# Kernel tuning notes

Measured on AMD Instinct MI355X. Metric: run time of the kernel, lower is better.

## Reference

```python
import jax, jax.numpy as jnp
import numpy as np
import math

T, B, E, H = 1024, 4, 512, 8
HD = E // H

def setup_inputs() -> dict:
    key = jax.random.key(0)
    ks = jax.random.split(key, 6)
    return {
        "query": jax.random.normal(ks[0], (T, B, E), dtype=jnp.float32),
        "dist": jax.random.normal(ks[1], (B, T, T, H), dtype=jnp.float32) * 0.1,
        "in_proj_weight": jax.random.normal(ks[2], (3 * E, E), dtype=jnp.float32) * 0.02,
        "in_proj_bias": jax.random.normal(ks[3], (3 * E,), dtype=jnp.float32) * 0.02,
        "out_proj_weight": jax.random.normal(ks[4], (E, E), dtype=jnp.float32) * 0.02,
        "out_proj_bias": jax.random.normal(ks[5], (E,), dtype=jnp.float32) * 0.02,
    }

def reference(query, dist, in_proj_weight, in_proj_bias, out_proj_weight, out_proj_bias):
    t, b, e = query.shape
    # packed in-projection (self-attention: q=k=v=query)
    qkv = query @ in_proj_weight.T + in_proj_bias          # [T,B,3E]
    q, k, v = jnp.split(qkv, 3, axis=-1)                   # each [T,B,E]
    def heads(x):
        return x.reshape(t, b * H, HD).transpose(1, 0, 2)  # [B*H,T,HD]
    q, k, v = heads(q), heads(k), heads(v)
    q = q / math.sqrt(HD)
    attn = jnp.einsum('bte,bse->bts', q, k)                # [B*H,T,T]
    # distance/structure bias: [B,T,T,H] -> [B,H,T,T] -> [B*H,T,T]
    bias = jnp.transpose(dist, (0, 3, 1, 2)).reshape(b * H, t, t)
    attn = jax.nn.softmax(attn + bias, axis=-1)
    out = jnp.einsum('bts,bse->bte', attn, v)              # [B*H,T,HD]
    out = out.transpose(1, 0, 2).reshape(t, b, e)          # [T,B,E]
    out = out @ out_proj_weight.T + out_proj_bias
    return out
```

## Files before the change

kernel.cpp:

```cpp
#include <hip/hip_runtime.h>
#include <math.h>

typedef __bf16 bf16;
typedef bf16 bf16x8 __attribute__((ext_vector_type(8)));
typedef bf16 bf16x4 __attribute__((ext_vector_type(4)));
typedef float f32x4 __attribute__((ext_vector_type(4)));

#define T_DIM 1024
#define B_DIM 4
#define E_DIM 512
#define H_DIM 8
#define HD_DIM 64
#define BH_DIM 32

__device__ __forceinline__ f32x4 mfma16(bf16x8 a, bf16x8 b, f32x4 c) {
    return __builtin_amdgcn_mfma_f32_16x16x32_bf16(a, b, c, 0, 0, 0);
}

__device__ __forceinline__ bf16x4 cvt4(f32x4 v) {
    bf16x4 o;
    o[0] = (bf16)v[0]; o[1] = (bf16)v[1]; o[2] = (bf16)v[2]; o[3] = (bf16)v[3];
    return o;
}

__global__ __launch_bounds__(256)
void bias_transpose(const float* __restrict__ dist, bf16* __restrict__ bias_t) {
    const int bt = blockIdx.x;
    const int b = bt >> 10, t = bt & 1023;
    const float* src = dist + ((long)bt << 13);
    const int tid = threadIdx.x;
#pragma unroll
    for (int rep = 0; rep < 4; rep++) {
        int slot = rep * 256 + tid;
        int h = slot >> 7;
        int sc = (slot & 127) * 8;
        bf16x8 o;
#pragma unroll
        for (int i = 0; i < 8; i++)
            o[i] = (bf16)src[(sc + i) * 8 + h];
        *(bf16x8*)&bias_t[((long)(b * 8 + h) * T_DIM + t) * T_DIM + sc] = o;
    }
}

template<int TM, int TN, int MODE>
__global__ __launch_bounds__(256)
void gemm_t(const float* __restrict__ A, const float* __restrict__ Bt,
            const float* __restrict__ bias, int K, int N,
            float* __restrict__ out, bf16* __restrict__ qb,
            bf16* __restrict__ kb, bf16* __restrict__ vb) {
    constexpr int FM = TM / 32, FN = TN / 32;
    __shared__ __align__(16) bf16 As[TM * 72];
    __shared__ __align__(16) bf16 Bs[TN * 72];
    const int tid  = threadIdx.x;
    const int lane = tid & 63;
    const int wave = tid >> 6;
    const int quad = lane >> 4;
    const int l15  = lane & 15;
    const int wm = wave & 1, wn = wave >> 1;
    const int m0 = blockIdx.x * TM, n0 = blockIdx.y * TN;

    f32x4 acc[FM][FN] = {};

    const int sr = tid >> 2;
    const int sc = (tid & 3) * 16;

    for (int k0 = 0; k0 < K; k0 += 64) {
#pragma unroll
        for (int p = 0; p < TM / 64; p++) {
            const float* src = &A[(long)(m0 + p * 64 + sr) * K + k0 + sc];
#pragma unroll
            for (int j = 0; j < 4; j++)
                *(bf16x4*)&As[(p * 64 + sr) * 72 + sc + j * 4] =
                    cvt4(*(const f32x4*)(src + j * 4));
        }
#pragma unroll
        for (int p = 0; p < TN / 64; p++) {
            const float* src = &Bt[(long)(n0 + p * 64 + sr) * K + k0 + sc];
#pragma unroll
            for (int j = 0; j < 4; j++)
                *(bf16x4*)&Bs[(p * 64 + sr) * 72 + sc + j * 4] =
                    cvt4(*(const f32x4*)(src + j * 4));
        }
        __syncthreads();
#pragma unroll
        for (int kk = 0; kk < 64; kk += 32) {
            bf16x8 af[FM], bf[FN];
#pragma unroll
            for (int mb = 0; mb < FM; mb++)
                af[mb] = *(const bf16x8*)&As[(wm * (TM / 2) + mb * 16 + l15) * 72 + kk + quad * 8];
#pragma unroll
            for (int nb = 0; nb < FN; nb++)
                bf[nb] = *(const bf16x8*)&Bs[(wn * (TN / 2) + nb * 16 + l15) * 72 + kk + quad * 8];
#pragma unroll
            for (int mb = 0; mb < FM; mb++)
#pragma unroll
                for (int nb = 0; nb < FN; nb++)
                    acc[mb][nb] = mfma16(af[mb], bf[nb], acc[mb][nb]);
        }
        __syncthreads();
    }

#pragma unroll
    for (int mb = 0; mb < FM; mb++) {
#pragma unroll
        for (int nb = 0; nb < FN; nb++) {
            int n = n0 + wn * (TN / 2) + nb * 16 + l15;
            float bv = bias[n];
#pragma unroll
            for (int r = 0; r < 4; r++) {
                int m = m0 + wm * (TM / 2) + mb * 16 + quad * 4 + r;
                float v = acc[mb][nb][r] + bv;
                if (MODE == 0) {
                    out[(long)m * N + n] = v;
                } else {
                    int t = m >> 2, b = m & 3;
                    int sec = n >> 9, j = n & 511;
                    int h = j >> 6, hd = j & 63;
                    int bh = b * 8 + h;
                    if (sec == 0)
                        qb[((long)bh * T_DIM + t) * HD_DIM + hd] = (bf16)(v * 0.125f);
                    else if (sec == 1)
                        kb[((long)bh * T_DIM + t) * HD_DIM + hd] = (bf16)v;
                    else
                        vb[((long)bh * HD_DIM + hd) * T_DIM + t] = (bf16)v;
                }
            }
        }
    }
}

__global__ __launch_bounds__(256)
void attn_kernel(const bf16* __restrict__ qb, const bf16* __restrict__ kb,
                 const bf16* __restrict__ vb, const bf16* __restrict__ bias_t,
                 float* __restrict__ ctx) {
    __shared__ __align__(16) bf16 Ks[64 * 72];
    __shared__ __align__(16) bf16 Vts[64 * 72];
    __shared__ __align__(16) bf16 Bs[64 * 72];
    __shared__ __align__(16) bf16 Ps[4 * 16 * 72];
    const int tid  = threadIdx.x;
    const int lane = tid & 63;
    const int wave = tid >> 6;
    const int quad = lane >> 4;
    const int l15  = lane & 15;
    const int bid = blockIdx.x;
    const int bh  = bid >> 4;
    const int qt  = bid & 15;
    const int b   = bh >> 3, h = bh & 7;
    const int qrow = qt * 64 + wave * 16 + l15;

    bf16x8 qa0 = *(const bf16x8*)&qb[((long)bh * T_DIM + qrow) * HD_DIM + quad * 8];
    bf16x8 qa1 = *(const bf16x8*)&qb[((long)bh * T_DIM + qrow) * HD_DIM + 32 + quad * 8];

    f32x4 oacc[4] = {};
    float lsum[4] = {0.f, 0.f, 0.f, 0.f};

    const int r0 = tid >> 3;
    const int c0 = (tid & 7) * 8;

    const bf16* biasrow0 = &bias_t[((long)bh * T_DIM + qt * 64 + r0) * T_DIM];
    const bf16* biasrow1 = &bias_t[((long)bh * T_DIM + qt * 64 + r0 + 32) * T_DIM];

    bf16x8 pk0, pk1, pv0, pv1, pb0, pb1;
    pk0 = *(const bf16x8*)&kb[((long)bh * T_DIM + r0) * HD_DIM + c0];
    pk1 = *(const bf16x8*)&kb[((long)bh * T_DIM + r0 + 32) * HD_DIM + c0];
    pv0 = *(const bf16x8*)&vb[((long)bh * HD_DIM + r0) * T_DIM + c0];
    pv1 = *(const bf16x8*)&vb[((long)bh * HD_DIM + r0 + 32) * T_DIM + c0];
    pb0 = *(const bf16x8*)&biasrow0[c0];
    pb1 = *(const bf16x8*)&biasrow1[c0];

    for (int st = 0; st < T_DIM; st += 64) {
        __syncthreads();
        *(bf16x8*)&Ks[r0 * 72 + c0]         = pk0;
        *(bf16x8*)&Ks[(r0 + 32) * 72 + c0]  = pk1;
        *(bf16x8*)&Vts[r0 * 72 + c0]        = pv0;
        *(bf16x8*)&Vts[(r0 + 32) * 72 + c0] = pv1;
        *(bf16x8*)&Bs[r0 * 72 + c0]         = pb0;
        *(bf16x8*)&Bs[(r0 + 32) * 72 + c0]  = pb1;
        __syncthreads();

        if (st + 64 < T_DIM) {
            const int sn = st + 64;
            pk0 = *(const bf16x8*)&kb[((long)bh * T_DIM + sn + r0) * HD_DIM + c0];
            pk1 = *(const bf16x8*)&kb[((long)bh * T_DIM + sn + r0 + 32) * HD_DIM + c0];
            pv0 = *(const bf16x8*)&vb[((long)bh * HD_DIM + r0) * T_DIM + sn + c0];
            pv1 = *(const bf16x8*)&vb[((long)bh * HD_DIM + r0 + 32) * T_DIM + sn + c0];
            pb0 = *(const bf16x8*)&biasrow0[sn + c0];
            pb1 = *(const bf16x8*)&biasrow1[sn + c0];
        }

        f32x4 sacc[4] = {};
#pragma unroll
        for (int kk = 0; kk < 64; kk += 32) {
            bf16x8 a = (kk == 0) ? qa0 : qa1;
#pragma unroll
            for (int nb = 0; nb < 4; nb++) {
                bf16x8 bfr = *(const bf16x8*)&Ks[(nb * 16 + l15) * 72 + kk + quad * 8];
                sacc[nb] = mfma16(a, bfr, sacc[nb]);
            }
        }

        bf16* pw = &Ps[wave * 16 * 72];
#pragma unroll
        for (int r = 0; r < 4; r++) {
            const int tl = wave * 16 + quad * 4 + r;
            float rs = 0.f;
#pragma unroll
            for (int nb = 0; nb < 4; nb++) {
                float d = (float)Bs[tl * 72 + nb * 16 + l15];
                float p = __expf(sacc[nb][r] + d);
                rs += p;
                pw[(quad * 4 + r) * 72 + nb * 16 + l15] = (bf16)p;
            }
            lsum[r] += rs;
        }

#pragma unroll
        for (int kk = 0; kk < 64; kk += 32) {
            bf16x8 ap = *(const bf16x8*)&pw[l15 * 72 + kk + quad * 8];
#pragma unroll
            for (int nb = 0; nb < 4; nb++) {
                bf16x8 bv2 = *(const bf16x8*)&Vts[(nb * 16 + l15) * 72 + kk + quad * 8];
                oacc[nb] = mfma16(ap, bv2, oacc[nb]);
            }
        }
    }

#pragma unroll
    for (int r = 0; r < 4; r++) {
#pragma unroll
        for (int msk = 1; msk < 16; msk <<= 1)
            lsum[r] += __shfl_xor(lsum[r], msk);
    }

#pragma unroll
    for (int nb = 0; nb < 4; nb++) {
#pragma unroll
        for (int r = 0; r < 4; r++) {
            int t  = qt * 64 + wave * 16 + quad * 4 + r;
            int hd = nb * 16 + l15;
            float o = oacc[nb][r] / lsum[r];
            ctx[((long)t * B_DIM + b) * E_DIM + h * HD_DIM + hd] = o;
        }
    }
}

extern "C" void kernel_launch(void* const* d_in, const int* in_sizes, int n_in,
                              void* d_out, int out_size, void* d_ws, size_t ws_size,
                              hipStream_t stream) {
    const float* query = (const float*)d_in[0];
    const float* dist  = (const float*)d_in[1];
    const float* win   = (const float*)d_in[2];
    const float* bin   = (const float*)d_in[3];
    const float* wout  = (const float*)d_in[4];
    const float* bout  = (const float*)d_in[5];
    float* out = (float*)d_out;

    bf16* bias_t = (bf16*)d_ws;
    bf16* qb  = bias_t + ((long)BH_DIM * T_DIM * T_DIM);
    bf16* kb  = qb + (1 << 21);
    bf16* vb  = kb + (1 << 21);
    float* ctx = (float*)(vb + (1 << 21));

    bias_transpose<<<dim3(B_DIM * T_DIM), 256, 0, stream>>>(dist, bias_t);
    gemm_t<128, 128, 1><<<dim3(32, 12), 256, 0, stream>>>(
        query, win, bin, 512, 1536, nullptr, qb, kb, vb);
    attn_kernel<<<dim3(512), 256, 0, stream>>>(qb, kb, vb, bias_t, ctx);
    gemm_t<128, 64, 0><<<dim3(32, 8), 256, 0, stream>>>(
        ctx, wout, bout, 512, 512, out, nullptr, nullptr, nullptr);
}
```

Baseline: 321.9 us.

## Coalesce bias transpose via LDS and pre-convert GEMM operands to bf16

```diff
diff --git a/kernel.cpp b/kernel.cpp
--- a/kernel.cpp
+++ b/kernel.cpp
@@ -23,28 +23,55 @@
     return o;
 }
 
+#define CVT_Q_V   524288
+#define CVT_W1_V  196608
+__global__ __launch_bounds__(256)
+void cvt_all(const float* __restrict__ q, const float* __restrict__ w1,
+             const float* __restrict__ w2, bf16* __restrict__ qo,
+             bf16* __restrict__ w1o, bf16* __restrict__ w2o) {
+    long v = (long)blockIdx.x * 256 + threadIdx.x;
+    const float* src; bf16* dst;
+    if (v < CVT_Q_V)                { src = q;  dst = qo; }
+    else if (v < CVT_Q_V + CVT_W1_V){ v -= CVT_Q_V;  src = w1; dst = w1o; }
+    else                            { v -= CVT_Q_V + CVT_W1_V; src = w2; dst = w2o; }
+    f32x4 f = *(const f32x4*)(src + v * 4);
+    *(bf16x4*)(dst + v * 4) = cvt4(f);
+}
+
 __global__ __launch_bounds__(256)
 void bias_transpose(const float* __restrict__ dist, bf16* __restrict__ bias_t) {
+    __shared__ __align__(16) bf16 tile[8 * 1032];
     const int bt = blockIdx.x;
     const int b = bt >> 10, t = bt & 1023;
-    const float* src = dist + ((long)bt << 13);
     const int tid = threadIdx.x;
+    const float* src = dist + ((long)bt << 13) + tid * 32;
+    const int s0 = tid * 4;
+    float v[32];
+#pragma unroll
+    for (int j = 0; j < 8; j++) {
+        f32x4 f = *(const f32x4*)(src + j * 4);
+        v[j * 4 + 0] = f[0]; v[j * 4 + 1] = f[1];
+        v[j * 4 + 2] = f[2]; v[j * 4 + 3] = f[3];
+    }
+#pragma unroll
+    for (int h = 0; h < 8; h++)
+#pragma unroll
+        for (int si = 0; si < 4; si++)
+            tile[h * 1032 + s0 + si] = (bf16)v[si * 8 + h];
+    __syncthreads();
 #pragma unroll
     for (int rep = 0; rep < 4; rep++) {
         int slot = rep * 256 + tid;
         int h = slot >> 7;
         int sc = (slot & 127) * 8;
-        bf16x8 o;
-#pragma unroll
-        for (int i = 0; i < 8; i++)
-            o[i] = (bf16)src[(sc + i) * 8 + h];
+        bf16x8 o = *(const bf16x8*)&tile[h * 1032 + sc];
         *(bf16x8*)&bias_t[((long)(b * 8 + h) * T_DIM + t) * T_DIM + sc] = o;
     }
 }
 
 template<int TM, int TN, int MODE>
 __global__ __launch_bounds__(256)
-void gemm_t(const float* __restrict__ A, const float* __restrict__ Bt,
+void gemm_t(const bf16* __restrict__ A, const bf16* __restrict__ Bt,
             const float* __restrict__ bias, int K, int N,
             float* __restrict__ out, bf16* __restrict__ qb,
             bf16* __restrict__ kb, bf16* __restrict__ vb) {
@@ -67,19 +94,15 @@
     for (int k0 = 0; k0 < K; k0 += 64) {
 #pragma unroll
         for (int p = 0; p < TM / 64; p++) {
-            const float* src = &A[(long)(m0 + p * 64 + sr) * K + k0 + sc];
-#pragma unroll
-            for (int j = 0; j < 4; j++)
-                *(bf16x4*)&As[(p * 64 + sr) * 72 + sc + j * 4] =
-                    cvt4(*(const f32x4*)(src + j * 4));
+            const bf16* src = &A[(long)(m0 + p * 64 + sr) * K + k0 + sc];
+            *(bf16x8*)&As[(p * 64 + sr) * 72 + sc]     = *(const bf16x8*)(src);
+            *(bf16x8*)&As[(p * 64 + sr) * 72 + sc + 8] = *(const bf16x8*)(src + 8);
         }
 #pragma unroll
         for (int p = 0; p < TN / 64; p++) {
-            const float* src = &Bt[(long)(n0 + p * 64 + sr) * K + k0 + sc];
-#pragma unroll
-            for (int j = 0; j < 4; j++)
-                *(bf16x4*)&Bs[(p * 64 + sr) * 72 + sc + j * 4] =
-                    cvt4(*(const f32x4*)(src + j * 4));
+            const bf16* src = &Bt[(long)(n0 + p * 64 + sr) * K + k0 + sc];
+            *(bf16x8*)&Bs[(p * 64 + sr) * 72 + sc]     = *(const bf16x8*)(src);
+            *(bf16x8*)&Bs[(p * 64 + sr) * 72 + sc + 8] = *(const bf16x8*)(src + 8);
         }
         __syncthreads();
 #pragma unroll
@@ -244,6 +267,13 @@
     }
 }
 
+__global__ __launch_bounds__(256)
+void cvt_ctx(const float* __restrict__ src, bf16* __restrict__ dst) {
+    long v = (long)blockIdx.x * 256 + threadIdx.x;
+    f32x4 f = *(const f32x4*)(src + v * 4);
+    *(bf16x4*)(dst + v * 4) = cvt4(f);
+}
+
 extern "C" void kernel_launch(void* const* d_in, const int* in_sizes, int n_in,
                               void* d_out, int out_size, void* d_ws, size_t ws_size,
                               hipStream_t stream) {
@@ -256,15 +286,21 @@
     float* out = (float*)d_out;
 
     bf16* bias_t = (bf16*)d_ws;
-    bf16* qb  = bias_t + ((long)BH_DIM * T_DIM * T_DIM);
-    bf16* kb  = qb + (1 << 21);
-    bf16* vb  = kb + (1 << 21);
+    bf16* qb   = bias_t + ((long)BH_DIM * T_DIM * T_DIM);
+    bf16* kb   = qb + (1 << 21);
+    bf16* vb   = kb + (1 << 21);
     float* ctx = (float*)(vb + (1 << 21));
-
+    bf16* qbf  = (bf16*)(ctx + (1 << 21));
+    bf16* w1bf = qbf + (1 << 21);
+    bf16* w2bf = w1bf + 786432;
+    bf16* ctxb = w2bf + 262144;
+
+    cvt_all<<<dim3(3072), 256, 0, stream>>>(query, win, wout, qbf, w1bf, w2bf);
     bias_transpose<<<dim3(B_DIM * T_DIM), 256, 0, stream>>>(dist, bias_t);
     gemm_t<128, 128, 1><<<dim3(32, 12), 256, 0, stream>>>(
-        query, win, bin, 512, 1536, nullptr, qb, kb, vb);
+        qbf, w1bf, bin, 512, 1536, nullptr, qb, kb, vb);
     attn_kernel<<<dim3(512), 256, 0, stream>>>(qb, kb, vb, bias_t, ctx);
+    cvt_ctx<<<dim3(2048), 256, 0, stream>>>(ctx, ctxb);
     gemm_t<128, 64, 0><<<dim3(32, 8), 256, 0, stream>>>(
-        ctx, wout, bout, 512, 512, out, nullptr, nullptr, nullptr);
-}
+        ctxb, w2bf, bout, 512, 512, out, nullptr, nullptr, nullptr);
+}
```

New measurement: 286.3 us. 11.1% less time.
